# Performance work log

Measured on AMD Instinct MI355X. Metric: run time of the kernel, lower is better.

Reference implementation:

```python
import jax, jax.numpy as jnp
import numpy as np

B, N, D = 16, 1024, 768
H = 12
HD = D // H
HID = 4 * D
EPS = 1e-6


def _layernorm(x, g, b):
    mu = jnp.mean(x, axis=-1, keepdims=True)
    var = jnp.mean(jnp.square(x - mu), axis=-1, keepdims=True)
    return (x - mu) * jax.lax.rsqrt(var + EPS) * g + b


def setup_inputs() -> dict:
    key = jax.random.key(0)
    ks = jax.random.split(key, 8)
    s_d = 1.0 / np.sqrt(D)
    s_h = 1.0 / np.sqrt(HID)
    return {
        "x": jax.random.normal(ks[0], (B, N, D), dtype=jnp.float32),
        "qkv_w": jax.random.uniform(ks[1], (3 * D, D), jnp.float32, -s_d, s_d),
        "proj_w": jax.random.uniform(ks[2], (D, D), jnp.float32, -s_d, s_d),
        "proj_b": jax.random.uniform(ks[3], (D,), jnp.float32, -s_d, s_d),
        "fc1_w": jax.random.uniform(ks[4], (HID, D), jnp.float32, -s_d, s_d),
        "fc1_b": jax.random.uniform(ks[5], (HID,), jnp.float32, -s_d, s_d),
        "fc2_w": jax.random.uniform(ks[6], (D, HID), jnp.float32, -s_h, s_h),
        "fc2_b": jax.random.uniform(ks[7], (D,), jnp.float32, -s_h, s_h),
        "norm1_g": jnp.ones((D,), jnp.float32),
        "norm1_b": jnp.zeros((D,), jnp.float32),
        "norm2_g": jnp.ones((D,), jnp.float32),
        "norm2_b": jnp.zeros((D,), jnp.float32),
    }


def _attention(x, qkv_w, proj_w, proj_b):
    b, n, _ = x.shape
    qkv = x @ qkv_w.T                                  # [b,n,3D] (no bias: qkv_bias=False)
    qkv = qkv.reshape(b, n, 3, H, HD)
    q, k, v = (jnp.transpose(qkv[:, :, i], (0, 2, 1, 3)) for i in range(3))  # [b,h,n,hd]
    scale = HD ** (-0.5)
    dots = jnp.einsum("bhid,bhjd->bhij", q, k) * scale
    attn = jax.nn.softmax(dots, axis=-1)
    out = jnp.einsum("bhij,bhjd->bhid", attn, v)
    out = jnp.transpose(out, (0, 2, 1, 3)).reshape(b, n, H * HD)
    return out @ proj_w.T + proj_b


def _mlp(x, fc1_w, fc1_b, fc2_w, fc2_b):
    h = jax.nn.gelu(x @ fc1_w.T + fc1_b, approximate=False)
    return h @ fc2_w.T + fc2_b


def reference(x, qkv_w, proj_w, proj_b, fc1_w, fc1_b, fc2_w, fc2_b,
              norm1_g, norm1_b, norm2_g, norm2_b):
    x = x + _attention(_layernorm(x, norm1_g, norm1_b), qkv_w, proj_w, proj_b)
    x = x + _mlp(_layernorm(x, norm2_g, norm2_b), fc1_w, fc1_b, fc2_w, fc2_b)
    return x
```

## Files before the change

### kernel.cpp

```cpp
#include <hip/hip_runtime.h>
#include <hip/hip_bf16.h>
#include <math.h>

using bf16 = __hip_bfloat16;
typedef __attribute__((ext_vector_type(8))) short short8;
typedef __attribute__((ext_vector_type(4))) short shortx4;
typedef __attribute__((ext_vector_type(4))) float floatx4;

#define BB 16
#define NN 1024
#define DD 768
#define HH 12
#define HD 64
#define HID 3072

__device__ __forceinline__ floatx4 mfma_bf16(short8 a, short8 b, floatx4 c) {
  return __builtin_amdgcn_mfma_f32_16x16x32_bf16(a, b, c, 0, 0, 0);
}

__device__ __forceinline__ short bf16_bits(float f) {
  union { bf16 h; short s; } u;
  u.h = __float2bfloat16(f);
  return u.s;
}

__device__ __forceinline__ void async_copy16(const void* g, void* l) {
  __builtin_amdgcn_global_load_lds(
      (const __attribute__((address_space(1))) unsigned int*)g,
      (__attribute__((address_space(3))) unsigned int*)l,
      16, 0, 0);
}

__global__ __launch_bounds__(256)
void cvt_kernel(const float* __restrict__ in, bf16* __restrict__ out, int n4)
{
  const int i = blockIdx.x * 256 + threadIdx.x;
  if (i >= n4) return;
  const float4 v = ((const float4*)in)[i];
  shortx4 o;
  o.x = bf16_bits(v.x); o.y = bf16_bits(v.y);
  o.z = bf16_bits(v.z); o.w = bf16_bits(v.w);
  ((shortx4*)out)[i] = o;
}

__global__ __launch_bounds__(256)
void ln_kernel(const float* __restrict__ x, const float* __restrict__ g,
               const float* __restrict__ b, bf16* __restrict__ y)
{
  const int row = blockIdx.x;
  const int t = threadIdx.x;
  const float* xr = x + (size_t)row * DD;
  float v[3];
  float s = 0.f, s2 = 0.f;
#pragma unroll
  for (int i = 0; i < 3; ++i) {
    float f = xr[t + i * 256];
    v[i] = f;
    s += f;
    s2 += f * f;
  }
#pragma unroll
  for (int off = 1; off < 64; off <<= 1) {
    s  += __shfl_xor(s, off);
    s2 += __shfl_xor(s2, off);
  }
  __shared__ float red[2][4];
  const int wave = t >> 6, lane = t & 63;
  if (lane == 0) { red[0][wave] = s; red[1][wave] = s2; }
  __syncthreads();
  s  = red[0][0] + red[0][1] + red[0][2] + red[0][3];
  s2 = red[1][0] + red[1][1] + red[1][2] + red[1][3];
  const float mu = s * (1.f / DD);
  const float var = s2 * (1.f / DD) - mu * mu;
  const float inv = rsqrtf(var + 1e-6f);
  bf16* yr = y + (size_t)row * DD;
#pragma unroll
  for (int i = 0; i < 3; ++i) {
    int c = t + i * 256;
    yr[c] = __float2bfloat16((v[i] - mu) * inv * g[c] + b[c]);
  }
}

template <int EPI>
__global__ __launch_bounds__(256, 2)
void gemm_kernel(const bf16* __restrict__ A, const bf16* __restrict__ W,
                 const float* __restrict__ bias, const float* __restrict__ res,
                 void* __restrict__ Cv, int N, int K)
{
  __shared__ __align__(16) short sA[128 * 64];
  __shared__ __align__(16) short sB[128 * 64];

  const int tid  = threadIdx.x;
  const int lane = tid & 63;
  const int wave = tid >> 6;
  const int wm = wave & 1, wn = wave >> 1;
  const int row16 = lane & 15, quad = lane >> 4;
  const int bm = blockIdx.y * 128, bn = blockIdx.x * 128;

  const int lrow = lane >> 3;
  const int lkc  = (lane & 7) ^ lrow;

  const bf16* Ag = A + (size_t)(bm + wave * 32 + lrow) * K + lkc * 8;
  const bf16* Bg = W + (size_t)(bn + wave * 32 + lrow) * K + lkc * 8;
  short* sAw = sA + wave * 2048;
  short* sBw = sB + wave * 2048;

  floatx4 acc[4][4] = {};

  for (int kt = 0; kt < K; kt += 64) {
#pragma unroll
    for (int g = 0; g < 4; ++g) {
      async_copy16(Ag + (size_t)g * 8 * K + kt, sAw + g * 512);
      async_copy16(Bg + (size_t)g * 8 * K + kt, sBw + g * 512);
    }
    __syncthreads();
#pragma unroll
    for (int c = 0; c < 2; ++c) {
      short8 af[4], bfr[4];
      const int kc = c * 4 + quad;
#pragma unroll
      for (int mt = 0; mt < 4; ++mt) {
        const int row = wm * 64 + mt * 16 + row16;
        af[mt] = *(const short8*)&sA[(row >> 3) * 512 + ((row & 7) * 8 + (kc ^ (row & 7))) * 8];
      }
#pragma unroll
      for (int nt = 0; nt < 4; ++nt) {
        const int row = wn * 64 + nt * 16 + row16;
        bfr[nt] = *(const short8*)&sB[(row >> 3) * 512 + ((row & 7) * 8 + (kc ^ (row & 7))) * 8];
      }
#pragma unroll
      for (int mt = 0; mt < 4; ++mt)
#pragma unroll
        for (int nt = 0; nt < 4; ++nt)
          acc[mt][nt] = mfma_bf16(af[mt], bfr[nt], acc[mt][nt]);
    }
    __syncthreads();
  }

  const int crow0 = bm + wm * 64;
  const int ccol0 = bn + wn * 64;
#pragma unroll
  for (int nt = 0; nt < 4; ++nt) {
    const int col = ccol0 + nt * 16 + row16;
    float bv = 0.f;
    if (EPI != 0) bv = bias[col];
#pragma unroll
    for (int mt = 0; mt < 4; ++mt) {
#pragma unroll
      for (int r = 0; r < 4; ++r) {
        const int row = crow0 + mt * 16 + quad * 4 + r;
        float v = acc[mt][nt][r] + bv;
        if (EPI == 1) {
          v += res[(size_t)row * N + col];
          ((float*)Cv)[(size_t)row * N + col] = v;
        } else {
          if (EPI == 2) v = 0.5f * v * (1.f + erff(v * 0.70710678118f));
          ((bf16*)Cv)[(size_t)row * N + col] = __float2bfloat16(v);
        }
      }
    }
  }
}

__global__ __launch_bounds__(256)
void vtrans_kernel(const bf16* __restrict__ qkv, bf16* __restrict__ vt)
{
  const int bh = blockIdx.y;
  const int b = bh / HH, h = bh % HH;
  const int n0 = blockIdx.x * 64;
  __shared__ __align__(16) short tile[64 * 72];
  const int tid = threadIdx.x;

  const int r = tid >> 2, c16 = (tid & 3) * 16;
  const bf16* src = qkv + (size_t)(b * NN + n0 + r) * 2304 + 2 * DD + h * 64 + c16;
  *(short8*)&tile[r * 72 + c16]     = *(const short8*)(src);
  *(short8*)&tile[r * 72 + c16 + 8] = *(const short8*)(src + 8);
  __syncthreads();

#pragma unroll
  for (int it = 0; it < 2; ++it) {
    const int d  = (tid >> 3) + it * 32;
    const int jg = (tid & 7) * 8;
    short8 o;
#pragma unroll
    for (int t = 0; t < 8; ++t) ((short*)&o)[t] = tile[(jg + t) * 72 + d];
    *(short8*)&vt[((size_t)bh * 64 + d) * NN + n0 + jg] = o;
  }
}

__global__ __launch_bounds__(256, 2)
void attn_kernel(const bf16* __restrict__ qkv, const bf16* __restrict__ vt,
                 bf16* __restrict__ out)
{
  const int bh = blockIdx.y;
  const int b = bh / HH, h = bh % HH;
  const int q0 = blockIdx.x * 128;
  const int tid = threadIdx.x;
  const int lane = tid & 63;
  const int wave = tid >> 6;
  const int row16 = lane & 15, quad = lane >> 4;

  __shared__ __align__(16) short sK[64 * 72];
  __shared__ __align__(16) short sVt[64 * 72];
  __shared__ __align__(16) short sP[4][32 * 72];

  const bf16* base  = qkv + (size_t)b * NN * 2304 + h * 64;
  const bf16* vbase = vt + (size_t)bh * 64 * NN;

  short8 qf[2][2];
#pragma unroll
  for (int qg = 0; qg < 2; ++qg) {
    const bf16* qrow = base + (size_t)(q0 + wave * 32 + qg * 16 + row16) * 2304;
    qf[qg][0] = *(const short8*)(qrow + quad * 8);
    qf[qg][1] = *(const short8*)(qrow + 32 + quad * 8);
  }

  floatx4 o_acc[2][4] = {};
  floatx4 l_acc[2] = {};
  const short8 ones = { (short)0x3F80, (short)0x3F80, (short)0x3F80, (short)0x3F80,
                        (short)0x3F80, (short)0x3F80, (short)0x3F80, (short)0x3F80 };

  const int sr = tid >> 2;
  const int sc = (tid & 3) * 16;

  const float ESC = 0.1803368801f;

  for (int jt = 0; jt < NN / 64; ++jt) {
    const int j0 = jt * 64;
    {
      const bf16* kp = base + (size_t)(j0 + sr) * 2304 + DD + sc;
      *(short8*)&sK[sr * 72 + sc]     = *(const short8*)(kp);
      *(short8*)&sK[sr * 72 + sc + 8] = *(const short8*)(kp + 8);
      const bf16* vp = vbase + (size_t)sr * NN + j0 + sc;
      *(short8*)&sVt[sr * 72 + sc]     = *(const short8*)(vp);
      *(short8*)&sVt[sr * 72 + sc + 8] = *(const short8*)(vp + 8);
    }
    __syncthreads();

#pragma unroll
    for (int nt = 0; nt < 4; ++nt) {
      short8 kb0 = *(const short8*)&sK[(nt * 16 + row16) * 72 + quad * 8];
      short8 kb1 = *(const short8*)&sK[(nt * 16 + row16) * 72 + 32 + quad * 8];
#pragma unroll
      for (int qg = 0; qg < 2; ++qg) {
        floatx4 st = {};
        st = mfma_bf16(kb0, qf[qg][0], st);
        st = mfma_bf16(kb1, qf[qg][1], st);
        shortx4 pk;
#pragma unroll
        for (int r = 0; r < 4; ++r)
          pk[r] = bf16_bits(exp2f(fminf(st[r] * ESC, 30.f)));
        *(shortx4*)&sP[wave][(qg * 16 + row16) * 72 + nt * 16 + quad * 4] = pk;
      }
    }

    short8 vb[4][2];
#pragma unroll
    for (int dt = 0; dt < 4; ++dt) {
      vb[dt][0] = *(const short8*)&sVt[(dt * 16 + row16) * 72 + quad * 8];
      vb[dt][1] = *(const short8*)&sVt[(dt * 16 + row16) * 72 + 32 + quad * 8];
    }
#pragma unroll
    for (int qg = 0; qg < 2; ++qg) {
      short8 pf0 = *(const short8*)&sP[wave][(qg * 16 + row16) * 72 + quad * 8];
      short8 pf1 = *(const short8*)&sP[wave][(qg * 16 + row16) * 72 + 32 + quad * 8];
      l_acc[qg] = mfma_bf16(pf0, ones, l_acc[qg]);
      l_acc[qg] = mfma_bf16(pf1, ones, l_acc[qg]);
#pragma unroll
      for (int dt = 0; dt < 4; ++dt) {
        o_acc[qg][dt] = mfma_bf16(pf0, vb[dt][0], o_acc[qg][dt]);
        o_acc[qg][dt] = mfma_bf16(pf1, vb[dt][1], o_acc[qg][dt]);
      }
    }
    __syncthreads();
  }

#pragma unroll
  for (int qg = 0; qg < 2; ++qg) {
#pragma unroll
    for (int r = 0; r < 4; ++r) {
      const float inv = 1.f / l_acc[qg][r];
      const size_t n = (size_t)(b * NN + q0 + wave * 32 + qg * 16 + quad * 4 + r);
#pragma unroll
      for (int dt = 0; dt < 4; ++dt) {
        out[n * DD + h * 64 + dt * 16 + row16] =
            __float2bfloat16(o_acc[qg][dt][r] * inv);
      }
    }
  }
}

extern "C" void kernel_launch(void* const* d_in, const int* in_sizes, int n_in,
                              void* d_out, int out_size, void* d_ws, size_t ws_size,
                              hipStream_t stream)
{
  const float* x       = (const float*)d_in[0];
  const float* qkv_w   = (const float*)d_in[1];
  const float* proj_w  = (const float*)d_in[2];
  const float* proj_b  = (const float*)d_in[3];
  const float* fc1_w   = (const float*)d_in[4];
  const float* fc1_b   = (const float*)d_in[5];
  const float* fc2_w   = (const float*)d_in[6];
  const float* fc2_b   = (const float*)d_in[7];
  const float* norm1_g = (const float*)d_in[8];
  const float* norm1_b = (const float*)d_in[9];
  const float* norm2_g = (const float*)d_in[10];
  const float* norm2_b = (const float*)d_in[11];
  float* out = (float*)d_out;

  const int M = BB * NN;
  char* ws = (char*)d_ws;

  bf16* wq = (bf16*)ws;
  bf16* wp = wq + (size_t)3 * DD * DD;
  bf16* w1 = wp + (size_t)DD * DD;
  bf16* w2 = w1 + (size_t)HID * DD;
  bf16* xn = w2 + (size_t)DD * HID;
  char* p2 = (char*)(xn + (size_t)M * DD);
  const size_t base_b = (size_t)(p2 - ws);

  int NBc = 1;
  for (int c = 16; c >= 1; c >>= 1)
    if (ws_size >= base_b + (size_t)c * 1024 * 7680) { NBc = c; break; }

  const int Rc = NBc * NN;
  bf16* qkvb = (bf16*)p2;
  bf16* aob  = qkvb + (size_t)Rc * 2304;
  bf16* vtb  = aob  + (size_t)Rc * DD;
  bf16* hb   = (bf16*)p2;

  cvt_kernel<<<(3 * DD * DD / 4 + 255) / 256, 256, 0, stream>>>(qkv_w, wq, 3 * DD * DD / 4);
  cvt_kernel<<<(DD * DD / 4 + 255) / 256, 256, 0, stream>>>(proj_w, wp, DD * DD / 4);
  cvt_kernel<<<(HID * DD / 4 + 255) / 256, 256, 0, stream>>>(fc1_w, w1, HID * DD / 4);
  cvt_kernel<<<(DD * HID / 4 + 255) / 256, 256, 0, stream>>>(fc2_w, w2, DD * HID / 4);

  ln_kernel<<<M, 256, 0, stream>>>(x, norm1_g, norm1_b, xn);

  for (int c = 0; c < BB / NBc; ++c) {
    const size_t r0 = (size_t)c * Rc;
    gemm_kernel<0><<<dim3(3 * DD / 128, Rc / 128), 256, 0, stream>>>(
        xn + r0 * DD, wq, nullptr, nullptr, qkvb, 3 * DD, DD);
    vtrans_kernel<<<dim3(NN / 64, NBc * HH), 256, 0, stream>>>(qkvb, vtb);
    attn_kernel<<<dim3(NN / 128, NBc * HH), 256, 0, stream>>>(qkvb, vtb, aob);
    gemm_kernel<1><<<dim3(DD / 128, Rc / 128), 256, 0, stream>>>(
        aob, wp, proj_b, x + r0 * DD, out + r0 * DD, DD, DD);
  }

  ln_kernel<<<M, 256, 0, stream>>>(out, norm2_g, norm2_b, xn);

  for (int c = 0; c < BB / NBc; ++c) {
    const size_t r0 = (size_t)c * Rc;
    gemm_kernel<2><<<dim3(HID / 128, Rc / 128), 256, 0, stream>>>(
        xn + r0 * DD, w1, fc1_b, nullptr, hb, HID, DD);
    gemm_kernel<1><<<dim3(DD / 128, Rc / 128), 256, 0, stream>>>(
        hb, w2, fc2_b, out + r0 * DD, out + r0 * DD, DD, HID);
  }
}
```

Before: 601.3 us.

## Vectorize GEMM epilogue via swapped MFMA operands, LDS staging, and grouped tile order

The GEMM swaps the MFMA operand order so each lane holds four consecutive output columns. This lets the residual epilogue use float4 loads and stores, and the bf16 epilogues stage results through shared memory for 16-byte coalesced stores. Blocks are remapped into panels of eight row tiles to improve L2 reuse of weights, and launch bounds are raised to 4 blocks per CU. The risk is register pressure from the higher occupancy target, extra LDS traffic, and an added barrier in the epilogue.

```diff
diff --git a/kernel.cpp b/kernel.cpp
--- a/kernel.cpp
+++ b/kernel.cpp
@@ -82,20 +82,26 @@
 }
 
 template <int EPI>
-__global__ __launch_bounds__(256, 2)
+__global__ __launch_bounds__(256, 4)
 void gemm_kernel(const bf16* __restrict__ A, const bf16* __restrict__ W,
                  const float* __restrict__ bias, const float* __restrict__ res,
                  void* __restrict__ Cv, int N, int K)
 {
-  __shared__ __align__(16) short sA[128 * 64];
-  __shared__ __align__(16) short sB[128 * 64];
+  __shared__ __align__(16) short smem[16896];
+  short* sA = smem;
+  short* sB = smem + 8192;
 
   const int tid  = threadIdx.x;
   const int lane = tid & 63;
   const int wave = tid >> 6;
   const int wm = wave & 1, wn = wave >> 1;
   const int row16 = lane & 15, quad = lane >> 4;
-  const int bm = blockIdx.y * 128, bn = blockIdx.x * 128;
+
+  const int lin = blockIdx.y * gridDim.x + blockIdx.x;
+  const int per = gridDim.x * 8;
+  const int pan = lin / per, rem = lin % per;
+  const int bm = (pan * 8 + (rem & 7)) * 128;
+  const int bn = (rem >> 3) * 128;
 
   const int lrow = lane >> 3;
   const int lkc  = (lane & 7) ^ lrow;
@@ -132,32 +138,53 @@
       for (int mt = 0; mt < 4; ++mt)
 #pragma unroll
         for (int nt = 0; nt < 4; ++nt)
-          acc[mt][nt] = mfma_bf16(af[mt], bfr[nt], acc[mt][nt]);
-    }
-    __syncthreads();
-  }
-
-  const int crow0 = bm + wm * 64;
-  const int ccol0 = bn + wn * 64;
-#pragma unroll
-  for (int nt = 0; nt < 4; ++nt) {
-    const int col = ccol0 + nt * 16 + row16;
-    float bv = 0.f;
-    if (EPI != 0) bv = bias[col];
+          acc[mt][nt] = mfma_bf16(bfr[nt], af[mt], acc[mt][nt]);
+    }
+    __syncthreads();
+  }
+
+  if (EPI == 1) {
 #pragma unroll
     for (int mt = 0; mt < 4; ++mt) {
-#pragma unroll
-      for (int r = 0; r < 4; ++r) {
-        const int row = crow0 + mt * 16 + quad * 4 + r;
-        float v = acc[mt][nt][r] + bv;
-        if (EPI == 1) {
-          v += res[(size_t)row * N + col];
-          ((float*)Cv)[(size_t)row * N + col] = v;
-        } else {
+      const int row = bm + wm * 64 + mt * 16 + row16;
+#pragma unroll
+      for (int nt = 0; nt < 4; ++nt) {
+        const int col = bn + wn * 64 + nt * 16 + quad * 4;
+        const floatx4 bv = *(const floatx4*)&bias[col];
+        const floatx4 rv = *(const floatx4*)&res[(size_t)row * N + col];
+        floatx4 o;
+#pragma unroll
+        for (int r = 0; r < 4; ++r) o[r] = acc[mt][nt][r] + bv[r] + rv[r];
+        *(floatx4*)&((float*)Cv)[(size_t)row * N + col] = o;
+      }
+    }
+  } else {
+    short* sC = smem;
+#pragma unroll
+    for (int mt = 0; mt < 4; ++mt) {
+      const int lr = wm * 64 + mt * 16 + row16;
+#pragma unroll
+      for (int nt = 0; nt < 4; ++nt) {
+        const int lc = wn * 64 + nt * 16 + quad * 4;
+        floatx4 bv = {};
+        if (EPI == 2) bv = *(const floatx4*)&bias[bn + lc];
+        shortx4 pk;
+#pragma unroll
+        for (int r = 0; r < 4; ++r) {
+          float v = acc[mt][nt][r] + bv[r];
           if (EPI == 2) v = 0.5f * v * (1.f + erff(v * 0.70710678118f));
-          ((bf16*)Cv)[(size_t)row * N + col] = __float2bfloat16(v);
+          pk[r] = bf16_bits(v);
         }
-      }
+        *(shortx4*)&sC[lr * 132 + lc] = pk;
+      }
+    }
+    __syncthreads();
+#pragma unroll
+    for (int it = 0; it < 8; ++it) {
+      const int row = (tid >> 4) + it * 16;
+      const int col = (tid & 15) * 8;
+      short8 v = *(const short8*)&sC[row * 132 + col];
+      *(short8*)&((bf16*)Cv)[(size_t)(bm + row) * N + bn + col] = v;
     }
   }
 }
@@ -222,7 +249,6 @@
 
   const int sr = tid >> 2;
   const int sc = (tid & 3) * 16;
-
   const float ESC = 0.1803368801f;
 
   for (int jt = 0; jt < NN / 64; ++jt) {
```

Measured after the change: 567.0 us. 1.06x faster.
